# Kernel tuning notes

Measured on AMD Instinct MI355X. Metric: run time of the kernel, lower is better.

Reference implementation:

```python
import jax, jax.numpy as jnp
import numpy as np

B, S, D = 32, 4096, 512

def setup_inputs() -> dict:
    key = jax.random.key(0)
    ks = jax.random.split(key, 5)
    scale = 1.0 / np.sqrt(D)
    return {
        "query": jax.random.normal(ks[0], (B, D), jnp.float32),
        "values": jax.random.normal(ks[1], (B, S, D), jnp.float32),
        "W1": jax.random.normal(ks[2], (D, D), jnp.float32) * scale,
        "b1": jnp.zeros((D,), jnp.float32),
        "W2": jax.random.normal(ks[3], (D, D), jnp.float32) * scale,
        "b2": jnp.zeros((D,), jnp.float32),
        "V": jax.random.normal(ks[4], (D, 1), jnp.float32) * scale,
        "bv": jnp.zeros((1,), jnp.float32),
    }

def reference(query, values, W1, b1, W2, b2, V, bv):
    # query: [B, D], values: [B, S, D]
    q_proj = query @ W1 + b1                      # [B, D]
    v_proj = jnp.einsum('bsd,de->bse', values, W2) + b2  # [B, S, D]
    hidden = jnp.tanh(q_proj[:, None, :] + v_proj)       # [B, S, D]
    score = jnp.einsum('bsd,de->bse', hidden, V) + bv    # [B, S, 1]
    attn = jax.nn.softmax(score, axis=1)                 # softmax over seq axis
    context = jnp.sum(attn * values, axis=1)             # [B, D]
    return (context, attn)
```

## Files before the change

kernel.cpp:

```cpp
#include <hip/hip_runtime.h>
#include <hip/hip_bf16.h>
#include <stdint.h>

#define NB 32
#define NS 4096
#define ND 512

typedef __attribute__((ext_vector_type(8))) short short8;
typedef __attribute__((ext_vector_type(4))) float floatx4;
typedef __attribute__((ext_vector_type(4))) unsigned int uint4v;

__device__ __forceinline__ short f2bf(float f) {
    unsigned int u = __builtin_bit_cast(unsigned int, f);
    return (short)((u + 0x8000u) >> 16);
}

__device__ __forceinline__ unsigned int cvt_pk_bf16(float lo, float hi) {
    unsigned int r;
    asm("v_cvt_pk_bf16_f32 %0, %1, %2" : "=v"(r) : "v"(lo), "v"(hi));
    return r;
}

__device__ __forceinline__ float fast_tanh(float x) {
    float e = __expf(2.0f * x);
    return 1.0f - 2.0f * __builtin_amdgcn_rcpf(e + 1.0f);
}

__global__ void __launch_bounds__(256) qproj_kernel(
    const float* __restrict__ query, const float* __restrict__ W1,
    const float* __restrict__ b1, const float* __restrict__ b2,
    float* __restrict__ qb) {
    const int b  = blockIdx.x;
    const int es = blockIdx.y;
    const int t  = threadIdx.x;
    const int col = t & 63, kc = t >> 6;
    __shared__ float q[ND];
    __shared__ float red[256];
    q[t] = query[b * ND + t];
    q[t + 256] = query[b * ND + t + 256];
    __syncthreads();
    float acc = 0.f;
    const float* wp = W1 + (size_t)(kc * 128) * ND + es * 64 + col;
    const float* qp = q + kc * 128;
#pragma unroll 8
    for (int k = 0; k < 128; k++)
        acc += qp[k] * wp[(size_t)k * ND];
    red[t] = acc;
    __syncthreads();
    if (t < 64) {
        float s = red[t] + red[t + 64] + red[t + 128] + red[t + 192];
        int e = es * 64 + t;
        qb[b * ND + e] = s + b1[e] + b2[e];
    }
}

__global__ void __launch_bounds__(256) w2t_kernel(
    const float* __restrict__ W2, unsigned short* __restrict__ W2Tt) {
    int g = blockIdx.x * 256 + threadIdx.x;
    int nt = g >> 14;
    int ks = (g >> 10) & 15;
    int kq = (g >> 8) & 3;
    int n  = g & 255;
    int e  = nt * 256 + n;
    int k0 = ks * 32 + kq * 8;
    short8 v;
#pragma unroll
    for (int j = 0; j < 8; j++)
        v[j] = f2bf(W2[(size_t)(k0 + j) * ND + e]);
    *(short8*)&W2Tt[(size_t)g * 8] = v;
}

__global__ void __launch_bounds__(256, 3) scores_kernel(
    const float* __restrict__ values, const unsigned short* __restrict__ W2Tt,
    const float* __restrict__ qb, const float* __restrict__ V,
    float* __restrict__ pscores) {
    const int nt = blockIdx.x;
    const int st = blockIdx.y;
    const int b  = blockIdx.z;
    const int n0 = nt * 256, s0 = st * 64;

    __shared__ __align__(16) unsigned short sA[2][2048];
    __shared__ __align__(16) unsigned short sB[2][8192];
    __shared__ float sQb[256];
    __shared__ float sV[256];
    __shared__ float sRed[4][64];

    const int tid  = threadIdx.x;
    const int lane = tid & 63;
    const int wave = tid >> 6;
    const int mr = lane & 15;
    const int q  = lane >> 4;

    sQb[tid] = qb[b * ND + n0 + tid];
    sV[tid]  = V[n0 + tid];

    floatx4 acc[4][4] = {};

    const int arow = tid >> 2;
    const int ac   = tid & 3;
    const int ardo = arow * 32 + ((ac ^ ((tid >> 3) & 3)) * 8);
    const float* ag = values + ((size_t)b * NS + s0 + arow) * ND + ac * 8;

    const int afo = (q ^ ((mr >> 1) & 3)) * 8;

    const unsigned short* bbase = W2Tt + (size_t)(nt * 16) * 8192;

    float4 p0 = *(const float4*)(ag);
    float4 p1 = *(const float4*)(ag + 4);
    float4 arA0 = *(const float4*)(ag + 32);
    float4 arA1 = *(const float4*)(ag + 36);
#pragma unroll
    for (int r = 0; r < 4; r++) {
        int c = tid + 256 * r;
        __builtin_amdgcn_global_load_lds(
            (const __attribute__((address_space(1))) unsigned int*)(bbase + c * 8),
            (__attribute__((address_space(3))) unsigned int*)&sB[0][c * 8],
            16, 0, 0);
    }
    {
        uint4v w;
        w.x = cvt_pk_bf16(p0.x, p0.y); w.y = cvt_pk_bf16(p0.z, p0.w);
        w.z = cvt_pk_bf16(p1.x, p1.y); w.w = cvt_pk_bf16(p1.z, p1.w);
        *(uint4v*)&sA[0][ardo] = w;
    }
    __syncthreads();

#pragma unroll
    for (int ks = 0; ks < 16; ks++) {
        const int cur = ks & 1, nxt = cur ^ 1;

        short8 af[4], bfr[4];
#pragma unroll
        for (int i = 0; i < 4; i++)
            af[i] = *(const short8*)&sA[cur][(i * 16 + mr) * 32 + afo];
#pragma unroll
        for (int j = 0; j < 4; j++)
            bfr[j] = *(const short8*)&sB[cur][(q * 256 + wave * 64 + j * 16 + mr) * 8];

        if (ks < 15) {
            const unsigned short* bsrc = bbase + (size_t)(ks + 1) * 8192;
#pragma unroll
            for (int r = 0; r < 4; r++) {
                int c = tid + 256 * r;
                __builtin_amdgcn_global_load_lds(
                    (const __attribute__((address_space(1))) unsigned int*)(bsrc + c * 8),
                    (__attribute__((address_space(3))) unsigned int*)&sB[nxt][c * 8],
                    16, 0, 0);
            }
        }
        float4 n0v = {}, n1v = {};
        if (ks < 14) {
            n0v = *(const float4*)(ag + (ks + 2) * 32);
            n1v = *(const float4*)(ag + (ks + 2) * 32 + 4);
        }

#pragma unroll
        for (int i = 0; i < 4; i++)
#pragma unroll
            for (int j = 0; j < 4; j++)
                acc[i][j] = __builtin_amdgcn_mfma_f32_16x16x32_bf16(af[i], bfr[j], acc[i][j], 0, 0, 0);

        if (ks < 15) {
            uint4v w;
            w.x = cvt_pk_bf16(arA0.x, arA0.y); w.y = cvt_pk_bf16(arA0.z, arA0.w);
            w.z = cvt_pk_bf16(arA1.x, arA1.y); w.w = cvt_pk_bf16(arA1.z, arA1.w);
            *(uint4v*)&sA[nxt][ardo] = w;
        }
        arA0 = n0v; arA1 = n1v;

        __syncthreads();
    }

    float vcoef[4], qadd[4];
#pragma unroll
    for (int j = 0; j < 4; j++) {
        int col = wave * 64 + j * 16 + mr;
        vcoef[j] = sV[col];
        qadd[j]  = sQb[col];
    }

#pragma unroll
    for (int i = 0; i < 4; i++) {
#pragma unroll
        for (int r = 0; r < 4; r++) {
            float p = 0.f;
#pragma unroll
            for (int j = 0; j < 4; j++)
                p += fast_tanh(acc[i][j][r] + qadd[j]) * vcoef[j];
            p += __shfl_xor(p, 1);
            p += __shfl_xor(p, 2);
            p += __shfl_xor(p, 4);
            p += __shfl_xor(p, 8);
            if (mr == 0) sRed[wave][i * 16 + q * 4 + r] = p;
        }
    }
    __syncthreads();
    if (tid < 64) {
        float s = sRed[0][tid] + sRed[1][tid] + sRed[2][tid] + sRed[3][tid];
        pscores[((size_t)nt * NB + b) * NS + s0 + tid] = s;
    }
}

__global__ void __launch_bounds__(256) softmax_kernel(
    const float* __restrict__ pscores, float* __restrict__ attn) {
    int b = blockIdx.x;
    int t = threadIdx.x;
    __shared__ float red[4];
    __shared__ float bcast[2];
    const float* sc0 = pscores + (size_t)b * NS;
    const float* sc1 = pscores + (size_t)(NB + b) * NS;
    float v[16];
    float m = -1e30f;
#pragma unroll
    for (int i = 0; i < 16; i++) {
        v[i] = sc0[t + i * 256] + sc1[t + i * 256];
        m = fmaxf(m, v[i]);
    }
    for (int o = 32; o; o >>= 1) m = fmaxf(m, __shfl_xor(m, o));
    if ((t & 63) == 0) red[t >> 6] = m;
    __syncthreads();
    if (t == 0) bcast[0] = fmaxf(fmaxf(red[0], red[1]), fmaxf(red[2], red[3]));
    __syncthreads();
    m = bcast[0];
    float sum = 0.f;
#pragma unroll
    for (int i = 0; i < 16; i++) { v[i] = __expf(v[i] - m); sum += v[i]; }
    for (int o = 32; o; o >>= 1) sum += __shfl_xor(sum, o);
    if ((t & 63) == 0) red[t >> 6] = sum;
    __syncthreads();
    if (t == 0) bcast[1] = red[0] + red[1] + red[2] + red[3];
    __syncthreads();
    float inv = 1.0f / bcast[1];
    float* ao = attn + (size_t)b * NS;
#pragma unroll
    for (int i = 0; i < 16; i++) ao[t + i * 256] = v[i] * inv;
}

__global__ void __launch_bounds__(256) context_partial_kernel(
    const float* __restrict__ values, const float* __restrict__ attn,
    float* __restrict__ pctx) {
    int sc = blockIdx.x;
    int b  = blockIdx.y;
    int t  = threadIdx.x;
    __shared__ float sAttn[256];
    sAttn[t] = attn[(size_t)b * NS + sc * 256 + t];
    __syncthreads();
    int d = t * 2;
    const float2* vp = (const float2*)(values + ((size_t)b * NS + sc * 256) * ND + d);
    float ax = 0.f, ay = 0.f;
#pragma unroll 8
    for (int s = 0; s < 256; s++) {
        float a = sAttn[s];
        float2 v = vp[(size_t)s * 256];
        ax += a * v.x; ay += a * v.y;
    }
    pctx[((size_t)sc * 32 + b) * ND + d]     = ax;
    pctx[((size_t)sc * 32 + b) * ND + d + 1] = ay;
}

__global__ void __launch_bounds__(256) context_reduce_kernel(
    const float* __restrict__ pctx, float* __restrict__ ctx) {
    int i = blockIdx.x * 256 + threadIdx.x;
    float s = 0.f;
#pragma unroll
    for (int p = 0; p < 16; p++) s += pctx[(size_t)p * (32 * ND) + i];
    ctx[i] = s;
}

extern "C" void kernel_launch(void* const* d_in, const int* in_sizes, int n_in,
                              void* d_out, int out_size, void* d_ws, size_t ws_size,
                              hipStream_t stream) {
    const float* query  = (const float*)d_in[0];
    const float* values = (const float*)d_in[1];
    const float* W1     = (const float*)d_in[2];
    const float* b1     = (const float*)d_in[3];
    const float* W2     = (const float*)d_in[4];
    const float* b2     = (const float*)d_in[5];
    const float* V      = (const float*)d_in[6];

    float* ctx_out  = (float*)d_out;
    float* attn_out = (float*)d_out + NB * ND;

    char* ws = (char*)d_ws;
    float*          qb      = (float*)ws;
    unsigned short* W2Tt    = (unsigned short*)(ws + (64 << 10));
    float*          pscores = (float*)(ws + (576 << 10));
    float*          pctx    = pscores;

    qproj_kernel<<<dim3(NB, 8), 256, 0, stream>>>(query, W1, b1, b2, qb);
    w2t_kernel<<<128, 256, 0, stream>>>(W2, W2Tt);
    scores_kernel<<<dim3(2, 64, 32), 256, 0, stream>>>(values, W2Tt, qb, V, pscores);
    softmax_kernel<<<NB, 256, 0, stream>>>(pscores, attn_out);
    context_partial_kernel<<<dim3(16, 32), 256, 0, stream>>>(values, attn_out, pctx);
    context_reduce_kernel<<<64, 256, 0, stream>>>(pctx, ctx_out);
}
```

Baseline: 487.6 us.

## Load W2 fragments directly to registers, deepen A prefetch, vectorize context partial

The scores kernel drops the shared-memory staging of W2 tiles. Each wave now loads its B fragments straight from global memory into double-buffered registers, and the values prefetch is deepened to a three-stage register queue. The barrier is replaced by an explicit lgkmcnt wait plus s_barrier, and the MFMA block is wrapped in s_setprio. This frees LDS for higher occupancy and avoids the global-to-LDS-to-register round trip, at the cost of more VGPRs and redundant global reads of W2 across waves. The context partial kernel switches to float4 loads split across two row halves and combines them with a shared-memory reduction.

```diff
diff --git a/kernel.cpp b/kernel.cpp
--- a/kernel.cpp
+++ b/kernel.cpp
@@ -80,7 +80,6 @@
     const int n0 = nt * 256, s0 = st * 64;
 
     __shared__ __align__(16) unsigned short sA[2][2048];
-    __shared__ __align__(16) unsigned short sB[2][8192];
     __shared__ float sQb[256];
     __shared__ float sV[256];
     __shared__ float sRed[4][64];
@@ -103,72 +102,66 @@
 
     const int afo = (q ^ ((mr >> 1) & 3)) * 8;
 
-    const unsigned short* bbase = W2Tt + (size_t)(nt * 16) * 8192;
+    const unsigned short* bp = W2Tt + (size_t)nt * 16 * 8192 + (q * 256 + wave * 64 + mr) * 8;
 
     float4 p0 = *(const float4*)(ag);
     float4 p1 = *(const float4*)(ag + 4);
-    float4 arA0 = *(const float4*)(ag + 32);
-    float4 arA1 = *(const float4*)(ag + 36);
-#pragma unroll
-    for (int r = 0; r < 4; r++) {
-        int c = tid + 256 * r;
-        __builtin_amdgcn_global_load_lds(
-            (const __attribute__((address_space(1))) unsigned int*)(bbase + c * 8),
-            (__attribute__((address_space(3))) unsigned int*)&sB[0][c * 8],
-            16, 0, 0);
-    }
+    float4 aq[3][2];
+    aq[1][0] = *(const float4*)(ag + 32);  aq[1][1] = *(const float4*)(ag + 36);
+    aq[2][0] = *(const float4*)(ag + 64);  aq[2][1] = *(const float4*)(ag + 68);
+    short8 bq[2][4];
+#pragma unroll
+    for (int j = 0; j < 4; j++)
+        bq[0][j] = *(const short8*)(bp + j * 128);
     {
         uint4v w;
         w.x = cvt_pk_bf16(p0.x, p0.y); w.y = cvt_pk_bf16(p0.z, p0.w);
         w.z = cvt_pk_bf16(p1.x, p1.y); w.w = cvt_pk_bf16(p1.z, p1.w);
         *(uint4v*)&sA[0][ardo] = w;
     }
-    __syncthreads();
+    asm volatile("s_waitcnt lgkmcnt(0)" ::: "memory");
+    __builtin_amdgcn_s_barrier();
+    __builtin_amdgcn_sched_barrier(0);
 
 #pragma unroll
     for (int ks = 0; ks < 16; ks++) {
         const int cur = ks & 1, nxt = cur ^ 1;
 
-        short8 af[4], bfr[4];
+        short8 af[4];
 #pragma unroll
         for (int i = 0; i < 4; i++)
             af[i] = *(const short8*)&sA[cur][(i * 16 + mr) * 32 + afo];
-#pragma unroll
-        for (int j = 0; j < 4; j++)
-            bfr[j] = *(const short8*)&sB[cur][(q * 256 + wave * 64 + j * 16 + mr) * 8];
 
         if (ks < 15) {
-            const unsigned short* bsrc = bbase + (size_t)(ks + 1) * 8192;
-#pragma unroll
-            for (int r = 0; r < 4; r++) {
-                int c = tid + 256 * r;
-                __builtin_amdgcn_global_load_lds(
-                    (const __attribute__((address_space(1))) unsigned int*)(bsrc + c * 8),
-                    (__attribute__((address_space(3))) unsigned int*)&sB[nxt][c * 8],
-                    16, 0, 0);
-            }
-        }
-        float4 n0v = {}, n1v = {};
-        if (ks < 14) {
-            n0v = *(const float4*)(ag + (ks + 2) * 32);
-            n1v = *(const float4*)(ag + (ks + 2) * 32 + 4);
-        }
-
+            const float4 a0 = aq[(ks + 1) % 3][0], a1 = aq[(ks + 1) % 3][1];
+            uint4v w;
+            w.x = cvt_pk_bf16(a0.x, a0.y); w.y = cvt_pk_bf16(a0.z, a0.w);
+            w.z = cvt_pk_bf16(a1.x, a1.y); w.w = cvt_pk_bf16(a1.z, a1.w);
+            *(uint4v*)&sA[nxt][ardo] = w;
+        }
+
+        if (ks < 15) {
+            const unsigned short* bsrc = bp + (size_t)(ks + 1) * 8192;
+#pragma unroll
+            for (int j = 0; j < 4; j++)
+                bq[nxt][j] = *(const short8*)(bsrc + j * 128);
+        }
+        if (ks < 13) {
+            aq[ks % 3][0] = *(const float4*)(ag + (ks + 3) * 32);
+            aq[ks % 3][1] = *(const float4*)(ag + (ks + 3) * 32 + 4);
+        }
+
+        __builtin_amdgcn_s_setprio(1);
 #pragma unroll
         for (int i = 0; i < 4; i++)
 #pragma unroll
             for (int j = 0; j < 4; j++)
-                acc[i][j] = __builtin_amdgcn_mfma_f32_16x16x32_bf16(af[i], bfr[j], acc[i][j], 0, 0, 0);
-
-        if (ks < 15) {
-            uint4v w;
-            w.x = cvt_pk_bf16(arA0.x, arA0.y); w.y = cvt_pk_bf16(arA0.z, arA0.w);
-            w.z = cvt_pk_bf16(arA1.x, arA1.y); w.w = cvt_pk_bf16(arA1.z, arA1.w);
-            *(uint4v*)&sA[nxt][ardo] = w;
-        }
-        arA0 = n0v; arA1 = n1v;
-
-        __syncthreads();
+                acc[i][j] = __builtin_amdgcn_mfma_f32_16x16x32_bf16(af[i], bq[cur][j], acc[i][j], 0, 0, 0);
+        __builtin_amdgcn_s_setprio(0);
+
+        asm volatile("s_waitcnt lgkmcnt(0)" ::: "memory");
+        __builtin_amdgcn_s_barrier();
+        __builtin_amdgcn_sched_barrier(0);
     }
 
     float vcoef[4], qadd[4];
@@ -243,19 +236,26 @@
     int b  = blockIdx.y;
     int t  = threadIdx.x;
     __shared__ float sAttn[256];
+    __shared__ float4 sRed4[256];
     sAttn[t] = attn[(size_t)b * NS + sc * 256 + t];
     __syncthreads();
-    int d = t * 2;
-    const float2* vp = (const float2*)(values + ((size_t)b * NS + sc * 256) * ND + d);
-    float ax = 0.f, ay = 0.f;
+    const int half = t >> 7;
+    const int d0 = (t & 127) * 4;
+    const float* vp = values + ((size_t)b * NS + sc * 256 + half) * ND + d0;
+    float4 acc = {0.f, 0.f, 0.f, 0.f};
 #pragma unroll 8
-    for (int s = 0; s < 256; s++) {
-        float a = sAttn[s];
-        float2 v = vp[(size_t)s * 256];
-        ax += a * v.x; ay += a * v.y;
-    }
-    pctx[((size_t)sc * 32 + b) * ND + d]     = ax;
-    pctx[((size_t)sc * 32 + b) * ND + d + 1] = ay;
+    for (int s = 0; s < 128; s++) {
+        float a = sAttn[s * 2 + half];
+        float4 v = *(const float4*)(vp + (size_t)s * 2 * ND);
+        acc.x += a * v.x; acc.y += a * v.y; acc.z += a * v.z; acc.w += a * v.w;
+    }
+    sRed4[t] = acc;
+    __syncthreads();
+    if (t < 128) {
+        float4 r0 = sRed4[t], r1 = sRed4[t + 128];
+        float4 o = {r0.x + r1.x, r0.y + r1.y, r0.z + r1.z, r0.w + r1.w};
+        *(float4*)&pctx[((size_t)sc * 32 + b) * ND + d0] = o;
+    }
 }
 
 __global__ void __launch_bounds__(256) context_reduce_kernel(
```

New measurement: 465.7 us. -4.5%, faster.
